# Optimization experiments

Measured on AMD Instinct MI355X. Metric: run time of the kernel, lower is better.

Reference implementation:

```python
import jax, jax.numpy as jnp
import numpy as np

HID = 2048
NH = 16
NKV = 4
HD = 256
ROT = 64  # partial_rotary_factor 0.25 * 256
EPS = 1e-6
B, S = 2, 2048


def rms_norm(x, w, eps=EPS):
    # Qwen3.5 RMSNorm: zero-init weight, (1 + w) scaling, fp32 compute
    xf = x.astype(jnp.float32)
    out = xf * jax.lax.rsqrt(jnp.mean(xf * xf, axis=-1, keepdims=True) + eps)
    return (out * (1.0 + w.astype(jnp.float32))).astype(x.dtype)


def rotate_half(x):
    x1, x2 = jnp.split(x, 2, axis=-1)
    return jnp.concatenate([-x2, x1], axis=-1)


def apply_partial_rope(q, k, cos, sin):
    # q,k: [b,h,s,d]; cos,sin: [b,s,rot] -> unsqueeze head dim
    c = cos[:, None, :, :]
    s = sin[:, None, :, :]
    q_rot, q_pass = q[..., :ROT], q[..., ROT:]
    k_rot, k_pass = k[..., :ROT], k[..., ROT:]
    q_rot = q_rot * c + rotate_half(q_rot) * s
    k_rot = k_rot * c + rotate_half(k_rot) * s
    return (jnp.concatenate([q_rot, q_pass], -1), jnp.concatenate([k_rot, k_pass], -1))


def setup_inputs() -> dict:
    key = jax.random.key(0)
    ks = jax.random.split(key, 10)
    hidden_states = jax.random.normal(ks[0], (B, S, HID), jnp.float32)
    # rotary embeddings over ROT dims (half freqs duplicated, HF-style)
    inv_freq = 1.0 / (10000.0 ** (np.arange(0, ROT, 2, dtype=np.float32) / ROT))
    t = np.arange(S, dtype=np.float32)
    freqs = np.outer(t, inv_freq)  # [S, ROT/2]
    emb = np.concatenate([freqs, freqs], axis=-1)  # [S, ROT]
    cos = jnp.broadcast_to(jnp.cos(emb)[None], (B, S, ROT)).astype(jnp.float32)
    sin = jnp.broadcast_to(jnp.sin(emb)[None], (B, S, ROT)).astype(jnp.float32)
    # additive causal mask
    m = jnp.where(jnp.tril(jnp.ones((S, S), bool)), 0.0, -1e9).astype(jnp.float32)
    attention_mask = jnp.broadcast_to(m[None, None], (B, 1, S, S))
    sc = 0.02
    Wq = jax.random.normal(ks[1], (HID, NH * HD * 2), jnp.float32) * sc
    Wk = jax.random.normal(ks[2], (HID, NKV * HD), jnp.float32) * sc
    Wv = jax.random.normal(ks[3], (HID, NKV * HD), jnp.float32) * sc
    Wo = jax.random.normal(ks[4], (NH * HD, HID), jnp.float32) * sc
    q_norm_w = jax.random.normal(ks[5], (HD,), jnp.float32) * sc
    k_norm_w = jax.random.normal(ks[6], (HD,), jnp.float32) * sc
    Wr = jax.random.normal(ks[7], (HID, 2 * HD), jnp.float32) * sc  # dynamic router
    return {"hidden_states": hidden_states, "cos": cos, "sin": sin,
            "attention_mask": attention_mask, "Wq": Wq, "Wk": Wk, "Wv": Wv,
            "Wo": Wo, "q_norm_w": q_norm_w, "k_norm_w": k_norm_w, "Wr": Wr}


def reference(hidden_states, cos, sin, attention_mask, Wq, Wk, Wv, Wo, q_norm_w, k_norm_w, Wr):
    b, s, _ = hidden_states.shape
    # dynamic router -> per-token virtual gates (inner_head for q/k, inner_head_v for v)
    vectors = jax.nn.sigmoid(hidden_states @ Wr)           # [b,s,2*HD]
    g_qk, g_v = jnp.split(vectors, 2, axis=-1)             # [b,s,HD] each
    # fused q projection -> query + sigmoid output gate
    qkv = (hidden_states @ Wq).reshape(b, s, NH, 2 * HD)
    q, gate = jnp.split(qkv, 2, axis=-1)                   # [b,s,NH,HD]
    gate = gate.reshape(b, s, NH * HD)
    k = (hidden_states @ Wk).reshape(b, s, NKV, HD)
    v = (hidden_states @ Wv).reshape(b, s, NKV, HD)
    # per-head RMSNorm before RoPE
    q = rms_norm(q, q_norm_w)
    k = rms_norm(k, k_norm_w)
    q = q.transpose(0, 2, 1, 3)                            # [b,NH,s,HD]
    k = k.transpose(0, 2, 1, 3)                            # [b,NKV,s,HD]
    v = v.transpose(0, 2, 1, 3)
    # virtual gating (inner_head): per-token per-channel gate within each head
    q = q * g_qk[:, None, :, :]
    k = k * g_qk[:, None, :, :]
    v = v * g_v[:, None, :, :]
    # partial RoPE on first ROT dims
    q, k = apply_partial_rope(q, k, cos, sin)
    # GQA: repeat kv heads
    n_rep = NH // NKV
    k = jnp.repeat(k, n_rep, axis=1)                       # [b,NH,s,HD]
    v = jnp.repeat(v, n_rep, axis=1)
    scores = jnp.einsum('bhqd,bhkd->bhqk', q, k) / jnp.sqrt(jnp.float32(HD))
    scores = scores + attention_mask
    attn = jax.nn.softmax(scores.astype(jnp.float32), axis=-1).astype(q.dtype)
    out = jnp.einsum('bhqk,bhkd->bhqd', attn, v)
    out = out.transpose(0, 2, 1, 3).reshape(b, s, NH * HD)
    out = out * jax.nn.sigmoid(gate)                       # sigmoid output gate
    return out @ Wo
```

## Files before the change

kernel.cpp:

```cpp
#include <hip/hip_runtime.h>

#define S_LEN 2048
#define NB    2
#define NH    16
#define NKV   4
#define HDIM  256
#define LW    10752

using bf16x8 = __attribute__((ext_vector_type(8))) short;
using s16x4  = __attribute__((ext_vector_type(4))) short;
using f32x4  = __attribute__((ext_vector_type(4))) float;

__device__ __forceinline__ float bf2f(short u){
  union { float f; unsigned u; } x; x.u = ((unsigned)(unsigned short)u) << 16; return x.f;
}
__device__ __forceinline__ short f2bf(float f){
  unsigned i = __builtin_bit_cast(unsigned, f);
  unsigned r = (i + 0x7fffu + ((i >> 16) & 1u)) >> 16;
  return (short)r;
}
__device__ __forceinline__ float sigm(float x){ return 1.0f / (1.0f + __expf(-x)); }

__device__ __forceinline__ void gload16(const short* g, short* lds){
  __builtin_amdgcn_global_load_lds((const __attribute__((address_space(1))) void*)g,
                                   (__attribute__((address_space(3))) void*)lds,
                                   16, 0, 0);
}

__global__ void k_cvt(const float* __restrict__ in, short* __restrict__ out, int n4){
  int i = blockIdx.x * blockDim.x + threadIdx.x;
  if (i >= n4) return;
  float4 v = ((const float4*)in)[i];
  s16x4 o;
  o[0] = f2bf(v.x); o[1] = f2bf(v.y); o[2] = f2bf(v.z); o[3] = f2bf(v.w);
  ((s16x4*)out)[i] = o;
}

__global__ void k_wt(const float* __restrict__ Wq, const float* __restrict__ Wk,
                     const float* __restrict__ Wv, const float* __restrict__ Wr,
                     const float* __restrict__ Wo, short* __restrict__ WcatT,
                     short* __restrict__ WoT)
{
  __shared__ float tile[32][33];
  const int id = blockIdx.x;
  const float* src; short* dst; int R, C, Ct, local;
  if (id < 16384)      { src = Wq; dst = WcatT;                      R = 2048; C = 8192; Ct = 256; local = id; }
  else if (id < 18432) { src = Wk; dst = WcatT + (size_t)8192*2048;  R = 2048; C = 1024; Ct =  32; local = id - 16384; }
  else if (id < 20480) { src = Wv; dst = WcatT + (size_t)9216*2048;  R = 2048; C = 1024; Ct =  32; local = id - 18432; }
  else if (id < 21504) { src = Wr; dst = WcatT + (size_t)10240*2048; R = 2048; C =  512; Ct =  16; local = id - 20480; }
  else                 { src = Wo; dst = WoT;                        R = 4096; C = 2048; Ct =  64; local = id - 21504; }
  const int c0 = (local % Ct) * 32, r0 = (local / Ct) * 32;
  const int tx = threadIdx.x, ty = threadIdx.y;
  #pragma unroll
  for (int i = ty; i < 32; i += 8)
    tile[i][tx] = src[(size_t)(r0 + i) * C + c0 + tx];
  __syncthreads();
  #pragma unroll
  for (int i = ty; i < 32; i += 8)
    dst[(size_t)(c0 + i) * R + r0 + tx] = f2bf(tile[tx][i]);
}

__global__ void k_vt(const short* __restrict__ Ycat, short* __restrict__ VT){
  __shared__ short tile[32][33];
  int b = blockIdx.z >> 2, hk = blockIdx.z & 3;
  int s0 = blockIdx.x * 32, d0 = blockIdx.y * 32;
  int tx = threadIdx.x, ty = threadIdx.y;
  #pragma unroll
  for (int i = ty; i < 32; i += 8)
    tile[i][tx] = Ycat[(size_t)(b * S_LEN + s0 + i) * LW + 9216 + hk * 256 + d0 + tx];
  __syncthreads();
  #pragma unroll
  for (int i = ty; i < 32; i += 8)
    VT[(size_t)((b * NKV + hk) * HDIM + d0 + i) * S_LEN + s0 + tx] = tile[tx][i];
}

#define MFMA_(a, b, c) __builtin_amdgcn_mfma_f32_16x16x32_bf16(a, b, c, 0, 0, 0)
#define LDA_(buf, ks, mh, f) (*(const bf16x8*)&As[buf][ks][(wm*128 + (mh)*64 + (f)*16 + l15) * 32 + rdSlot])
#define LDB_(buf, ks, f)     (*(const bf16x8*)&Bs[buf][ks][(wn*64  + (f)*16 + l15) * 32 + rdSlot])
#define STAGE_A_(buf, ks, tile) { \
  gload16(aG0 + (size_t)(tile)*64 + (ks)*32, &As[buf][ks][w*512]); \
  gload16(aG1 + (size_t)(tile)*64 + (ks)*32, &As[buf][ks][4096 + w*512]); }
#define STAGE_B_(buf, ks, tile) { \
  gload16(bG0 + (size_t)(tile)*64 + (ks)*32, &Bs[buf][ks][w*512]); \
  gload16(bG1 + (size_t)(tile)*64 + (ks)*32, &Bs[buf][ks][4096 + w*512]); }
#define VM4 asm volatile("s_waitcnt vmcnt(4)" ::: "memory");
#define PH_(buf, ks, mh, LB, ...) { \
  bf16x8 a0 = LDA_(buf,ks,mh,0), a1 = LDA_(buf,ks,mh,1), a2 = LDA_(buf,ks,mh,2), a3 = LDA_(buf,ks,mh,3); \
  if (LB) { b0 = LDB_(buf,ks,0); b1 = LDB_(buf,ks,1); b2 = LDB_(buf,ks,2); b3 = LDB_(buf,ks,3); } \
  __VA_ARGS__ \
  __builtin_amdgcn_s_barrier(); \
  asm volatile("s_waitcnt lgkmcnt(0)" ::: "memory"); \
  __builtin_amdgcn_s_setprio(1); \
  acc[(mh)*4+0][0] = MFMA_(a0, b0, acc[(mh)*4+0][0]); \
  acc[(mh)*4+0][1] = MFMA_(a0, b1, acc[(mh)*4+0][1]); \
  acc[(mh)*4+0][2] = MFMA_(a0, b2, acc[(mh)*4+0][2]); \
  acc[(mh)*4+0][3] = MFMA_(a0, b3, acc[(mh)*4+0][3]); \
  acc[(mh)*4+1][0] = MFMA_(a1, b0, acc[(mh)*4+1][0]); \
  acc[(mh)*4+1][1] = MFMA_(a1, b1, acc[(mh)*4+1][1]); \
  acc[(mh)*4+1][2] = MFMA_(a1, b2, acc[(mh)*4+1][2]); \
  acc[(mh)*4+1][3] = MFMA_(a1, b3, acc[(mh)*4+1][3]); \
  acc[(mh)*4+2][0] = MFMA_(a2, b0, acc[(mh)*4+2][0]); \
  acc[(mh)*4+2][1] = MFMA_(a2, b1, acc[(mh)*4+2][1]); \
  acc[(mh)*4+2][2] = MFMA_(a2, b2, acc[(mh)*4+2][2]); \
  acc[(mh)*4+2][3] = MFMA_(a2, b3, acc[(mh)*4+2][3]); \
  acc[(mh)*4+3][0] = MFMA_(a3, b0, acc[(mh)*4+3][0]); \
  acc[(mh)*4+3][1] = MFMA_(a3, b1, acc[(mh)*4+3][1]); \
  acc[(mh)*4+3][2] = MFMA_(a3, b2, acc[(mh)*4+3][2]); \
  acc[(mh)*4+3][3] = MFMA_(a3, b3, acc[(mh)*4+3][3]); \
  __builtin_amdgcn_s_setprio(0); \
  __builtin_amdgcn_s_barrier(); }

template<int OUTF32, int CM>
__global__ __launch_bounds__(512) void k_gemm2(const short* __restrict__ A,
                                               const short* __restrict__ BT,
                                               void* __restrict__ C,
                                               int M, int N, int K, int gx)
{
  __shared__ __align__(16) short As[2][2][8192];
  __shared__ __align__(16) short Bs[2][2][8192];
  const int t = threadIdx.x, lane = t & 63, w = t >> 6;
  const int l15 = lane & 15;
  const int wm = w >> 2, wn = w & 3;
  const int rdSlot = (((lane >> 4) ^ ((lane >> 1) & 3)) * 8);

  const int nwg = gridDim.x;
  const int swz = (blockIdx.x & 7) * (nwg >> 3) + (blockIdx.x >> 3);
  const int m0 = (CM ? (swz % gx) : (swz / gx)) * 256;
  const int n0 = (CM ? (swz / gx) : (swz % gx)) * 256;

  const int sRow = w * 16 + (lane >> 2);
  const int sSwz = ((lane & 3) ^ ((lane >> 3) & 3)) * 8;
  const short* aG0 = A  + (size_t)(m0 + sRow) * K + sSwz;
  const short* aG1 = A  + (size_t)(m0 + 128 + sRow) * K + sSwz;
  const short* bG0 = BT + (size_t)(n0 + sRow) * K + sSwz;
  const short* bG1 = BT + (size_t)(n0 + 128 + sRow) * K + sSwz;

  f32x4 acc[8][4] = {};
  bf16x8 b0 = {}, b1 = {}, b2 = {}, b3 = {};

  STAGE_A_(0, 0, 0) STAGE_A_(0, 1, 0) STAGE_B_(0, 0, 0) STAGE_B_(0, 1, 0)
  STAGE_A_(1, 0, 1) STAGE_B_(1, 0, 1)
  asm volatile("s_waitcnt vmcnt(4)" ::: "memory");
  __builtin_amdgcn_s_barrier();

  const int nIt = K >> 7;
  for (int i = 0; i < nIt; ++i) {
    const int c = 2 * i;
    const bool st = (i + 1 < nIt);
    PH_(0, 0, 0, 1, STAGE_A_(1, 1, c + 1))
    PH_(0, 0, 1, 0, STAGE_B_(1, 1, c + 1))
    PH_(0, 1, 0, 1, if (st) STAGE_A_(0, 0, c + 2))
    PH_(0, 1, 1, 0, if (st) STAGE_B_(0, 0, c + 2) VM4)
    PH_(1, 0, 0, 1, if (st) STAGE_A_(0, 1, c + 2))
    PH_(1, 0, 1, 0, if (st) STAGE_B_(0, 1, c + 2))
    PH_(1, 1, 0, 1, if (st) STAGE_A_(1, 0, c + 3))
    PH_(1, 1, 1, 0, if (st) STAGE_B_(1, 0, c + 3) VM4)
  }

  #pragma unroll
  for (int ii = 0; ii < 8; ++ii)
    #pragma unroll
    for (int r = 0; r < 4; ++r) {
      const int row = m0 + wm * 128 + ii * 16 + (lane >> 4) * 4 + r;
      #pragma unroll
      for (int j = 0; j < 4; ++j) {
        const int col = n0 + wn * 64 + j * 16 + l15;
        const float v = acc[ii][j][r];
        if (OUTF32) ((float*)C)[(size_t)row * N + col] = v;
        else        ((short*)C)[(size_t)row * N + col] = f2bf(v);
      }
    }
}

__global__ __launch_bounds__(256) void k_post(short* __restrict__ Ycat,
    const float* __restrict__ cosb, const float* __restrict__ sinb,
    const float* __restrict__ qw, const float* __restrict__ kw)
{
  const int tok = blockIdx.x;
  const int lane = threadIdx.x & 63, w = threadIdx.x >> 6;
  const size_t rowb = (size_t)tok * LW;
  const int d0 = lane * 4;

  float gq[4], gv[4];
  {
    s16x4 a  = *(const s16x4*)&Ycat[rowb + 10240 + d0];
    s16x4 bq = *(const s16x4*)&Ycat[rowb + 10240 + 256 + d0];
    #pragma unroll
    for (int j = 0; j < 4; ++j){ gq[j] = sigm(bf2f(a[j])); gv[j] = sigm(bf2f(bq[j])); }
  }
  float c4[4] = {0,0,0,0}, s4[4] = {0,0,0,0};
  if (lane < 16) {
    float4 c = *(const float4*)&cosb[(size_t)tok * 64 + d0];
    float4 s = *(const float4*)&sinb[(size_t)tok * 64 + d0];
    c4[0]=c.x; c4[1]=c.y; c4[2]=c.z; c4[3]=c.w;
    s4[0]=s.x; s4[1]=s.y; s4[2]=s.z; s4[3]=s.w;
  }
  float4 qv4 = *(const float4*)&qw[d0];
  float4 kv4 = *(const float4*)&kw[d0];
  float qwa[4] = {qv4.x, qv4.y, qv4.z, qv4.w};
  float kwa[4] = {kv4.x, kv4.y, kv4.z, kv4.w};

  #pragma unroll
  for (int hi = 0; hi < 4; ++hi) {
    const int hh = w * 4 + hi;
    const size_t off = rowb + hh * 512 + d0;
    s16x4 v = *(const s16x4*)&Ycat[off];
    float x[4];
    #pragma unroll
    for (int j = 0; j < 4; ++j) x[j] = bf2f(v[j]);
    float ss = x[0]*x[0] + x[1]*x[1] + x[2]*x[2] + x[3]*x[3];
    #pragma unroll
    for (int o2 = 1; o2 < 64; o2 <<= 1) ss += __shfl_xor(ss, o2);
    float rr = rsqrtf(ss * (1.0f/256.0f) + 1e-6f);
    #pragma unroll
    for (int j = 0; j < 4; ++j) x[j] = x[j] * rr * (1.0f + qwa[j]) * gq[j];
    float p[4];
    #pragma unroll
    for (int j = 0; j < 4; ++j) p[j] = __shfl_xor(x[j], 8);
    if (lane < 8)       { for (int j = 0; j < 4; ++j) x[j] = x[j]*c4[j] - p[j]*s4[j]; }
    else if (lane < 16) { for (int j = 0; j < 4; ++j) x[j] = x[j]*c4[j] + p[j]*s4[j]; }
    s16x4 o;
    #pragma unroll
    for (int j = 0; j < 4; ++j) o[j] = f2bf(x[j]);
    *(s16x4*)&Ycat[off] = o;
  }
  {
    const size_t off = rowb + 8192 + w * 256 + d0;
    s16x4 v = *(const s16x4*)&Ycat[off];
    float x[4];
    #pragma unroll
    for (int j = 0; j < 4; ++j) x[j] = bf2f(v[j]);
    float ss = x[0]*x[0] + x[1]*x[1] + x[2]*x[2] + x[3]*x[3];
    #pragma unroll
    for (int o2 = 1; o2 < 64; o2 <<= 1) ss += __shfl_xor(ss, o2);
    float rr = rsqrtf(ss * (1.0f/256.0f) + 1e-6f);
    #pragma unroll
    for (int j = 0; j < 4; ++j) x[j] = x[j] * rr * (1.0f + kwa[j]) * gq[j];
    float p[4];
    #pragma unroll
    for (int j = 0; j < 4; ++j) p[j] = __shfl_xor(x[j], 8);
    if (lane < 8)       { for (int j = 0; j < 4; ++j) x[j] = x[j]*c4[j] - p[j]*s4[j]; }
    else if (lane < 16) { for (int j = 0; j < 4; ++j) x[j] = x[j]*c4[j] + p[j]*s4[j]; }
    s16x4 o;
    #pragma unroll
    for (int j = 0; j < 4; ++j) o[j] = f2bf(x[j]);
    *(s16x4*)&Ycat[off] = o;
  }
  {
    const size_t off = rowb + 9216 + w * 256 + d0;
    s16x4 v = *(const s16x4*)&Ycat[off];
    s16x4 o;
    #pragma unroll
    for (int j = 0; j < 4; ++j) o[j] = f2bf(bf2f(v[j]) * gv[j]);
    *(s16x4*)&Ycat[off] = o;
  }
}

#define ATT_STAGE(bb, jj) { \
  _Pragma("unroll") \
  for (int ri = 0; ri < 4; ++ri) \
    gload16(kSrc + (size_t)((jj) + ri*8) * LW, &Ks[bb][t*8 + ri*2048]); \
  _Pragma("unroll") \
  for (int ri = 0; ri < 4; ++ri) \
    gload16(vSrc + (jj) + (size_t)(ri*64) * S_LEN, &Vs[bb][t*8 + ri*2048]); }

__global__ __launch_bounds__(256) void k_attn(const short* __restrict__ Ycat,
                                              const short* __restrict__ VT,
                                              short* __restrict__ AO)
{
  __shared__ __align__(16) short Ks[2][8192];
  __shared__ __align__(16) short Vs[2][8192];
  __shared__ __align__(16) short Ps[4][512];

  const int t = threadIdx.x, lane = t & 63, w = t >> 6;
  const int l15 = lane & 15, g = lane >> 4;
  const int id = blockIdx.x;
  const int xcd = id & 7, widx = id >> 3;
  const int b = xcd >> 2, hk = xcd & 3;
  const int h = hk * 4 + (widx & 3);
  const int x = widx >> 2, qq = x & 7, jj = x >> 3;
  const int qsel = (jj == 0) ? 31 - qq : (jj == 1) ? 16 + qq : (jj == 2) ? 15 - qq : qq;
  const int q0 = qsel * 64;
  const int qg = q0 + w * 16 + l15;
  const float SC2 = 0.09016844f;

  bf16x8 qf[8];
  {
    const size_t qb = ((size_t)(b * S_LEN) + qg) * LW + h * 512 + g * 8;
    #pragma unroll
    for (int kk = 0; kk < 8; ++kk)
      qf[kk] = *(const bf16x8*)&Ycat[qb + kk * 32];
  }
  asm volatile("s_waitcnt vmcnt(0)" ::: "memory");

  const int kRow = t >> 5;
  const int kColS = ((((t & 31) * 16) ^ ((kRow & 7) << 4)) >> 1);
  const int vRow = t >> 2;
  const int vColS = ((((t & 3) * 16) ^ ((vRow & 3) << 4)) >> 1);
  const short* kSrc = Ycat + ((size_t)(b * S_LEN) + kRow) * LW + 8192 + hk * 256 + kColS;
  const short* vSrc = VT + ((size_t)((b * NKV + hk) * HDIM + vRow)) * S_LEN + vColS;

  f32x4 oacc[16] = {};
  float m_r = -1e30f, l_r = 0.0f;

  const int nt = (q0 >> 5) + 2;
  ATT_STAGE(0, 0)
  int buf = 0;
  char* Pw = (char*)Ps[w] + l15 * 64;
  const int pswz = (l15 & 3) << 4;

  for (int ti = 0; ti < nt; ++ti) {
    const int j0 = ti * 32;
    const int jn = (ti + 1 < nt) ? j0 + 32 : 0;
    ATT_STAGE(buf ^ 1, jn)
    asm volatile("s_waitcnt vmcnt(8)" ::: "memory");
    __builtin_amdgcn_s_barrier();

    if (j0 <= q0 + w * 16 + 15) {
      f32x4 sa[2] = {};
      #pragma unroll
      for (int kk = 0; kk < 8; ++kk) {
        #pragma unroll
        for (int c = 0; c < 2; ++c) {
          const int row = c * 16 + l15;
          bf16x8 kf = *(const bf16x8*)((const char*)Ks[buf] + row * 512
                       + ((kk * 64 + g * 16) ^ ((l15 & 7) << 4)));
          sa[c] = __builtin_amdgcn_mfma_f32_16x16x32_bf16(kf, qf[kk], sa[c], 0, 0, 0);
        }
      }
      float s[8];
      #pragma unroll
      for (int c = 0; c < 2; ++c)
        #pragma unroll
        for (int r = 0; r < 4; ++r) s[c * 4 + r] = sa[c][r];
      if (j0 + 31 > qg) {
        #pragma unroll
        for (int c = 0; c < 2; ++c)
          #pragma unroll
          for (int r = 0; r < 4; ++r)
            if (j0 + c * 16 + g * 4 + r > qg) s[c * 4 + r] = -1e30f;
      }
      float mx = s[0];
      #pragma unroll
      for (int i = 1; i < 8; ++i) mx = fmaxf(mx, s[i]);
      mx = fmaxf(mx, __shfl_xor(mx, 16));
      mx = fmaxf(mx, __shfl_xor(mx, 32));
      if (!__all(mx - m_r <= 128.0f)) {
        const float mnew = fmaxf(m_r, mx);
        const float alpha = exp2f((m_r - mnew) * SC2);
        l_r *= alpha;
        #pragma unroll
        for (int jb = 0; jb < 16; ++jb)
          #pragma unroll
          for (int r = 0; r < 4; ++r) oacc[jb][r] *= alpha;
        m_r = mnew;
      }
      float p[8], rs = 0.0f;
      #pragma unroll
      for (int i = 0; i < 8; ++i) { p[i] = exp2f((s[i] - m_r) * SC2); rs += p[i]; }
      rs += __shfl_xor(rs, 16);
      rs += __shfl_xor(rs, 32);
      l_r += rs;
      #pragma unroll
      for (int c = 0; c < 2; ++c) {
        uint2 u;
        u.x = (unsigned short)f2bf(p[c*4+0]) | ((unsigned)(unsigned short)f2bf(p[c*4+1]) << 16);
        u.y = (unsigned short)f2bf(p[c*4+2]) | ((unsigned)(unsigned short)f2bf(p[c*4+3]) << 16);
        *(uint2*)(Pw + ((c * 32 + 8 * g) ^ pswz)) = u;
      }
      bf16x8 pa = *(const bf16x8*)(Pw + ((16 * g) ^ pswz));
      #pragma unroll
      for (int jb = 0; jb < 16; ++jb) {
        const int vrow = jb * 16 + l15;
        bf16x8 vf = *(const bf16x8*)((const char*)Vs[buf] + vrow * 64
                     + ((16 * g) ^ ((l15 & 3) << 4)));
        oacc[jb] = __builtin_amdgcn_mfma_f32_16x16x32_bf16(vf, pa, oacc[jb], 0, 0, 0);
      }
    }
    __builtin_amdgcn_s_barrier();
    buf ^= 1;
  }
  asm volatile("s_waitcnt vmcnt(0)" ::: "memory");

  const float linv = 1.0f / l_r;
  const size_t gb = ((size_t)(b * S_LEN) + qg) * LW + h * 512 + 256;
  const size_t ob = ((size_t)(b * S_LEN) + qg) * 4096 + h * 256;
  #pragma unroll
  for (int jb = 0; jb < 16; ++jb) {
    const int d0 = jb * 16 + g * 4;
    s16x4 gt = *(const s16x4*)&Ycat[gb + d0];
    s16x4 o;
    #pragma unroll
    for (int r = 0; r < 4; ++r)
      o[r] = f2bf(oacc[jb][r] * linv * sigm(bf2f(gt[r])));
    *(s16x4*)&AO[ob + d0] = o;
  }
}

extern "C" void kernel_launch(void* const* d_in, const int* in_sizes, int n_in,
                              void* d_out, int out_size, void* d_ws, size_t ws_size,
                              hipStream_t stream) {
  const float* X    = (const float*)d_in[0];
  const float* cosb = (const float*)d_in[1];
  const float* sinb = (const float*)d_in[2];
  const float* Wq   = (const float*)d_in[4];
  const float* Wk   = (const float*)d_in[5];
  const float* Wv   = (const float*)d_in[6];
  const float* Wo   = (const float*)d_in[7];
  const float* qw   = (const float*)d_in[8];
  const float* kw   = (const float*)d_in[9];
  const float* Wr   = (const float*)d_in[10];

  short* Xb    = (short*)d_ws;
  short* WcatT = Xb    +  8388608;
  short* AO    = WcatT;
  short* WoT   = WcatT + 22020096;
  short* Ycat  = WoT   +  8388608;
  short* VT    = Ycat  + 44040192;

  dim3 tb(32, 8);
  k_cvt<<<8192, 256, 0, stream>>>(X, Xb, 2097152);
  k_wt<<<29696, tb, 0, stream>>>(Wq, Wk, Wv, Wr, Wo, WcatT, WoT);

  k_gemm2<0, 1><<<672, 512, 0, stream>>>(Xb, WcatT, Ycat, 4096, 10752, 2048, 16);
  k_post<<<4096, 256, 0, stream>>>(Ycat, cosb, sinb, qw, kw);
  k_vt<<<dim3(64, 8, 8), tb, 0, stream>>>(Ycat, VT);
  k_attn<<<1024, 256, 0, stream>>>(Ycat, VT, AO);
  k_gemm2<1, 0><<<128, 512, 0, stream>>>(AO, WoT, d_out, 4096, 2048, 4096, 8);
}
```

Measured before the change: 537.2 us.

## Split-K the output projection GEMM and stage epilogue through LDS for vectorized stores

Measured after the change: 502.2 us. -6.5%, faster.

```diff
diff --git a/kernel.cpp b/kernel.cpp
--- a/kernel.cpp
+++ b/kernel.cpp
@@ -34,6 +34,17 @@
   s16x4 o;
   o[0] = f2bf(v.x); o[1] = f2bf(v.y); o[2] = f2bf(v.z); o[3] = f2bf(v.w);
   ((s16x4*)out)[i] = o;
+}
+
+__global__ void k_add(const float* __restrict__ b, float* __restrict__ o, int n4){
+  int i = blockIdx.x * blockDim.x + threadIdx.x;
+  const int stride = gridDim.x * blockDim.x;
+  for (; i < n4; i += stride) {
+    float4 x = ((const float4*)o)[i];
+    float4 y = ((const float4*)b)[i];
+    float4 z = {x.x + y.x, x.y + y.y, x.z + y.z, x.w + y.w};
+    ((float4*)o)[i] = z;
+  }
 }
 
 __global__ void k_wt(const float* __restrict__ Wq, const float* __restrict__ Wk,
@@ -75,6 +86,8 @@
 }
 
 #define MFMA_(a, b, c) __builtin_amdgcn_mfma_f32_16x16x32_bf16(a, b, c, 0, 0, 0)
+#define As ((short(*)[2][8192])(SMEM))
+#define Bs ((short(*)[2][8192])(SMEM + 32768))
 #define LDA_(buf, ks, mh, f) (*(const bf16x8*)&As[buf][ks][(wm*128 + (mh)*64 + (f)*16 + l15) * 32 + rdSlot])
 #define LDB_(buf, ks, f)     (*(const bf16x8*)&Bs[buf][ks][(wn*64  + (f)*16 + l15) * 32 + rdSlot])
 #define STAGE_A_(buf, ks, tile) { \
@@ -110,14 +123,15 @@
   __builtin_amdgcn_s_setprio(0); \
   __builtin_amdgcn_s_barrier(); }
 
-template<int OUTF32, int CM>
+template<int OUTF32, int CM, int SPLITK>
 __global__ __launch_bounds__(512) void k_gemm2(const short* __restrict__ A,
                                                const short* __restrict__ BT,
-                                               void* __restrict__ C,
-                                               int M, int N, int K, int gx)
+                                               void* __restrict__ C0,
+                                               void* __restrict__ C1,
+                                               int M, int N, int Kpitch, int Klen,
+                                               int gx)
 {
-  __shared__ __align__(16) short As[2][2][8192];
-  __shared__ __align__(16) short Bs[2][2][8192];
+  __shared__ __align__(16) short SMEM[65536];
   const int t = threadIdx.x, lane = t & 63, w = t >> 6;
   const int l15 = lane & 15;
   const int wm = w >> 2, wn = w & 3;
@@ -125,15 +139,21 @@
 
   const int nwg = gridDim.x;
   const int swz = (blockIdx.x & 7) * (nwg >> 3) + (blockIdx.x >> 3);
-  const int m0 = (CM ? (swz % gx) : (swz / gx)) * 256;
-  const int n0 = (CM ? (swz / gx) : (swz % gx)) * 256;
+  int rem = swz, kOff = 0;
+  void* Cp = C0;
+  if (SPLITK) {
+    rem = swz & 127;
+    if (swz >> 7) { kOff = Klen; Cp = C1; }
+  }
+  const int m0 = (CM ? (rem % gx) : (rem / gx)) * 256;
+  const int n0 = (CM ? (rem / gx) : (rem % gx)) * 256;
 
   const int sRow = w * 16 + (lane >> 2);
   const int sSwz = ((lane & 3) ^ ((lane >> 3) & 3)) * 8;
-  const short* aG0 = A  + (size_t)(m0 + sRow) * K + sSwz;
-  const short* aG1 = A  + (size_t)(m0 + 128 + sRow) * K + sSwz;
-  const short* bG0 = BT + (size_t)(n0 + sRow) * K + sSwz;
-  const short* bG1 = BT + (size_t)(n0 + 128 + sRow) * K + sSwz;
+  const short* aG0 = A  + (size_t)(m0 + sRow) * Kpitch + kOff + sSwz;
+  const short* aG1 = A  + (size_t)(m0 + 128 + sRow) * Kpitch + kOff + sSwz;
+  const short* bG0 = BT + (size_t)(n0 + sRow) * Kpitch + kOff + sSwz;
+  const short* bG1 = BT + (size_t)(n0 + 128 + sRow) * Kpitch + kOff + sSwz;
 
   f32x4 acc[8][4] = {};
   bf16x8 b0 = {}, b1 = {}, b2 = {}, b3 = {};
@@ -143,7 +163,7 @@
   asm volatile("s_waitcnt vmcnt(4)" ::: "memory");
   __builtin_amdgcn_s_barrier();
 
-  const int nIt = K >> 7;
+  const int nIt = Klen >> 7;
   for (int i = 0; i < nIt; ++i) {
     const int c = 2 * i;
     const bool st = (i + 1 < nIt);
@@ -157,20 +177,47 @@
     PH_(1, 1, 1, 0, if (st) STAGE_B_(1, 0, c + 3) VM4)
   }
 
-  #pragma unroll
-  for (int ii = 0; ii < 8; ++ii)
-    #pragma unroll
-    for (int r = 0; r < 4; ++r) {
-      const int row = m0 + wm * 128 + ii * 16 + (lane >> 4) * 4 + r;
-      #pragma unroll
-      for (int j = 0; j < 4; ++j) {
-        const int col = n0 + wn * 64 + j * 16 + l15;
-        const float v = acc[ii][j][r];
-        if (OUTF32) ((float*)C)[(size_t)row * N + col] = v;
-        else        ((short*)C)[(size_t)row * N + col] = f2bf(v);
-      }
+  float* Cl = (float*)SMEM;
+  const int g = lane >> 4;
+  #pragma unroll
+  for (int ch = 0; ch < 4; ++ch) {
+    if (wm == (ch >> 1)) {
+      #pragma unroll
+      for (int ii2 = 0; ii2 < 4; ++ii2)
+        #pragma unroll
+        for (int j = 0; j < 4; ++j)
+          #pragma unroll
+          for (int r = 0; r < 4; ++r)
+            Cl[(ii2*16 + g*4 + r) * 260 + wn*64 + j*16 + l15] = acc[(ch & 1)*4 + ii2][j][r];
     }
-}
+    asm volatile("s_waitcnt lgkmcnt(0)" ::: "memory");
+    __builtin_amdgcn_s_barrier();
+    #pragma unroll
+    for (int p = 0; p < 4; ++p) {
+      const int row = (t >> 5) + p * 16;
+      const int c8 = (t & 31) * 8;
+      f32x4 v0 = *(const f32x4*)&Cl[row * 260 + c8];
+      f32x4 v1 = *(const f32x4*)&Cl[row * 260 + c8 + 4];
+      const int grow = m0 + ch * 64 + row;
+      if (OUTF32) {
+        *(f32x4*)&((float*)Cp)[(size_t)grow * N + n0 + c8]     = v0;
+        *(f32x4*)&((float*)Cp)[(size_t)grow * N + n0 + c8 + 4] = v1;
+      } else {
+        unsigned d0, d1, d2, d3;
+        asm("v_cvt_pk_bf16_f32 %0, %1, %2" : "=v"(d0) : "v"(v0[0]), "v"(v0[1]));
+        asm("v_cvt_pk_bf16_f32 %0, %1, %2" : "=v"(d1) : "v"(v0[2]), "v"(v0[3]));
+        asm("v_cvt_pk_bf16_f32 %0, %1, %2" : "=v"(d2) : "v"(v1[0]), "v"(v1[1]));
+        asm("v_cvt_pk_bf16_f32 %0, %1, %2" : "=v"(d3) : "v"(v1[2]), "v"(v1[3]));
+        uint4 u = {d0, d1, d2, d3};
+        *(uint4*)&((short*)Cp)[(size_t)grow * N + n0 + c8] = u;
+      }
+    }
+    asm volatile("s_waitcnt lgkmcnt(0)" ::: "memory");
+    __builtin_amdgcn_s_barrier();
+  }
+}
+#undef As
+#undef Bs
 
 __global__ __launch_bounds__(256) void k_post(short* __restrict__ Ycat,
     const float* __restrict__ cosb, const float* __restrict__ sinb,
@@ -417,14 +464,18 @@
   short* WoT   = WcatT + 22020096;
   short* Ycat  = WoT   +  8388608;
   short* VT    = Ycat  + 44040192;
+  float* P1    = (float*)Ycat;
 
   dim3 tb(32, 8);
   k_cvt<<<8192, 256, 0, stream>>>(X, Xb, 2097152);
   k_wt<<<29696, tb, 0, stream>>>(Wq, Wk, Wv, Wr, Wo, WcatT, WoT);
 
-  k_gemm2<0, 1><<<672, 512, 0, stream>>>(Xb, WcatT, Ycat, 4096, 10752, 2048, 16);
+  k_gemm2<0, 1, 0><<<672, 512, 0, stream>>>(Xb, WcatT, Ycat, nullptr,
+                                            4096, 10752, 2048, 2048, 16);
   k_post<<<4096, 256, 0, stream>>>(Ycat, cosb, sinb, qw, kw);
   k_vt<<<dim3(64, 8, 8), tb, 0, stream>>>(Ycat, VT);
   k_attn<<<1024, 256, 0, stream>>>(Ycat, VT, AO);
-  k_gemm2<1, 0><<<128, 512, 0, stream>>>(AO, WoT, d_out, 4096, 2048, 4096, 8);
-}
+  k_gemm2<1, 0, 1><<<256, 512, 0, stream>>>(AO, WoT, d_out, P1,
+                                            4096, 2048, 4096, 2048, 8);
+  k_add<<<2048, 256, 0, stream>>>(P1, (float*)d_out, 2097152);
+}
```
